# Performance work log

Measured on AMD Instinct MI355X. Metric: run time of the kernel, lower is better.

## Reference

```python
import jax, jax.numpy as jnp
import numpy as np

B, S, HID = 2, 2048, 2048
NH, NKV, HD = 32, 8, 64
N_REP = NH // NKV
SCALING = HD ** -0.5
NEG_INF = -1e9


def rotate_half(x):
    x1, x2 = x[..., : x.shape[-1] // 2], x[..., x.shape[-1] // 2 :]
    return jnp.concatenate((-x2, x1), axis=-1)


def setup_inputs() -> dict:
    key = jax.random.key(0)
    ks = jax.random.split(key, 5)
    hidden_states = jax.random.normal(ks[0], (B, S, HID), dtype=jnp.float32)
    # real RoPE tables, theta=10000
    inv_freq = 1.0 / (10000.0 ** (jnp.arange(0, HD, 2, dtype=jnp.float32) / HD))
    freqs = jnp.arange(S, dtype=jnp.float32)[:, None] * inv_freq[None, :]  # [S, HD/2]
    emb = jnp.concatenate((freqs, freqs), axis=-1)  # [S, HD]
    cos = jnp.broadcast_to(jnp.cos(emb)[None], (B, S, HD))
    sin = jnp.broadcast_to(jnp.sin(emb)[None], (B, S, HD))
    # additive causal mask [B, 1, S, S]
    causal = jnp.tril(jnp.ones((S, S), dtype=bool))
    attention_mask = jnp.where(causal, 0.0, NEG_INF).astype(jnp.float32)
    attention_mask = jnp.broadcast_to(attention_mask[None, None], (B, 1, S, S))
    std = 0.02
    Wq = jax.random.normal(ks[1], (NH * HD, HID), dtype=jnp.float32) * std
    Wk = jax.random.normal(ks[2], (NKV * HD, HID), dtype=jnp.float32) * std
    Wv = jax.random.normal(ks[3], (NKV * HD, HID), dtype=jnp.float32) * std
    Wo = jax.random.normal(ks[4], (HID, NH * HD), dtype=jnp.float32) * std
    return {"hidden_states": hidden_states, "cos": cos, "sin": sin,
            "attention_mask": attention_mask, "Wq": Wq, "Wk": Wk, "Wv": Wv, "Wo": Wo}


def reference(hidden_states, cos, sin, attention_mask, Wq, Wk, Wv, Wo):
    b, s, _ = hidden_states.shape
    # projections (nn.Linear: y = x @ W.T), split heads -> [b, h, s, d]
    q = jnp.einsum("bsh,oh->bso", hidden_states, Wq).reshape(b, s, NH, HD).transpose(0, 2, 1, 3)
    k = jnp.einsum("bsh,oh->bso", hidden_states, Wk).reshape(b, s, NKV, HD).transpose(0, 2, 1, 3)
    v = jnp.einsum("bsh,oh->bso", hidden_states, Wv).reshape(b, s, NKV, HD).transpose(0, 2, 1, 3)
    # RoPE (cos/sin unsqueezed at dim 1)
    c, sn = cos[:, None], sin[:, None]
    q = q * c + rotate_half(q) * sn
    k = k * c + rotate_half(k) * sn
    # GQA repeat_kv
    k = jnp.repeat(k, N_REP, axis=1)
    v = jnp.repeat(v, N_REP, axis=1)
    # eager attention: QK^T -> +mask -> fp32 softmax -> V
    logits = jnp.einsum("bhqd,bhkd->bhqk", q, k) * SCALING + attention_mask
    attn_weights = jax.nn.softmax(logits.astype(jnp.float32), axis=-1).astype(q.dtype)
    attn_out = jnp.einsum("bhqk,bhkd->bhqd", attn_weights, v)
    attn_out = attn_out.transpose(0, 2, 1, 3).reshape(b, s, NH * HD)
    out = jnp.einsum("bso,ho->bsh", attn_out, Wo)
    return out, attn_weights
```

## Files before the change

kernel.cpp:

```cpp
#include <hip/hip_runtime.h>
#include <hip/hip_bf16.h>


typedef __bf16 bf16;
typedef bf16 bf16x8 __attribute__((ext_vector_type(8)));
typedef bf16 bf16x4 __attribute__((ext_vector_type(4)));
typedef float f32x4 __attribute__((ext_vector_type(4)));

#define B_   2
#define S_   2048
#define HID_ 2048
#define NH_  32
#define NKV_ 8
#define HD_  64
#define TOK_ (B_*S_)
#define QKVN 3072

#define BAR_LGKM() do { asm volatile("s_waitcnt lgkmcnt(0)" ::: "memory"); \
                        __builtin_amdgcn_s_barrier(); } while (0)

__device__ __forceinline__ void gl_lds16(const bf16* g, bf16* l) {
  __builtin_amdgcn_global_load_lds(
      (const __attribute__((address_space(1))) unsigned int*)(g),
      (__attribute__((address_space(3))) unsigned int*)(l), 16, 0, 0);
}

__global__ __launch_bounds__(256) void cast_f32_bf16(const float* __restrict__ in,
                                                     bf16* __restrict__ out, int n4) {
  int i = blockIdx.x * 256 + threadIdx.x;
  if (i >= n4) return;
  f32x4 v = ((const f32x4*)in)[i];
  bf16x4 o;
  o[0] = (bf16)v[0]; o[1] = (bf16)v[1]; o[2] = (bf16)v[2]; o[3] = (bf16)v[3];
  ((bf16x4*)out)[i] = o;
}

__global__ __launch_bounds__(256) void cast_wqkv(const float* __restrict__ wq,
                                                 const float* __restrict__ wk,
                                                 const float* __restrict__ wv,
                                                 bf16* __restrict__ dst) {
  int i = blockIdx.x * 256 + threadIdx.x;
  const float* src; int off;
  if (i < 1048576)      { src = wq; off = i; }
  else if (i < 1310720) { src = wk; off = i - 1048576; }
  else                  { src = wv; off = i - 1310720; }
  f32x4 v = ((const f32x4*)src)[off];
  bf16x4 o;
  o[0] = (bf16)v[0]; o[1] = (bf16)v[1]; o[2] = (bf16)v[2]; o[3] = (bf16)v[3];
  ((bf16x4*)dst)[i] = o;
}

template<bool OUT_F32>
__global__ __launch_bounds__(256) void gemm_bt(const bf16* __restrict__ A,
                                               const bf16* __restrict__ Bm,
                                               void* __restrict__ Cout,
                                               int M, int N, int K) {
  __shared__ __align__(16) bf16 As[128 * 32];
  __shared__ __align__(16) bf16 Bs[128 * 32];
  const int tid  = threadIdx.x;
  const int wave = tid >> 6, lane = tid & 63;

  const int nwg = (int)(gridDim.x * gridDim.y);
  const int bid = (int)(blockIdx.y * gridDim.x + blockIdx.x);
  const int swz = (bid & 7) * (nwg >> 3) + (bid >> 3);
  const int bx = swz % (int)gridDim.x, by = swz / (int)gridDim.x;

  const int bm = by * 128, bn = bx * 128;
  const int wm = (wave >> 1) * 64, wn = (wave & 1) * 64;
  const int fr = lane & 15, fg = lane >> 4;

  const int r0   = wave * 32 + (lane >> 2);
  const int scol = (lane & 3) * 8;
  const bf16* ga0 = A  + (size_t)(bm + r0) * K + scol;
  const bf16* ga1 = ga0 + (size_t)16 * K;
  const bf16* gb0 = Bm + (size_t)(bn + r0) * K + scol;
  const bf16* gb1 = gb0 + (size_t)16 * K;
  bf16* lA0 = As + (wave * 32) * 32;
  bf16* lA1 = lA0 + 16 * 32;
  bf16* lB0 = Bs + (wave * 32) * 32;
  bf16* lB1 = lB0 + 16 * 32;

  f32x4 acc[4][4] = {};

  for (int k0 = 0; k0 < K; k0 += 32) {
    gl_lds16(ga0 + k0, lA0);
    gl_lds16(ga1 + k0, lA1);
    gl_lds16(gb0 + k0, lB0);
    gl_lds16(gb1 + k0, lB1);
    __syncthreads();
    bf16x8 af[4], bfv[4];
#pragma unroll
    for (int i = 0; i < 4; ++i) {
      af[i]  = *(const bf16x8*)&As[(wm + i * 16 + fr) * 32 + fg * 8];
      bfv[i] = *(const bf16x8*)&Bs[(wn + i * 16 + fr) * 32 + fg * 8];
    }
#pragma unroll
    for (int i = 0; i < 4; ++i)
#pragma unroll
      for (int j = 0; j < 4; ++j)
        acc[i][j] = __builtin_amdgcn_mfma_f32_16x16x32_bf16(af[i], bfv[j], acc[i][j], 0, 0, 0);
    __syncthreads();
  }

#pragma unroll
  for (int i = 0; i < 4; ++i)
#pragma unroll
    for (int j = 0; j < 4; ++j)
#pragma unroll
      for (int r = 0; r < 4; ++r) {
        int row = bm + wm + i * 16 + fg * 4 + r;
        int col = bn + wn + j * 16 + fr;
        float v = acc[i][j][r];
        if (OUT_F32) ((float*)Cout)[(size_t)row * N + col] = v;
        else         ((bf16*)Cout)[(size_t)row * N + col] = (bf16)v;
      }
}

__global__ __launch_bounds__(256) void rope_fused(bf16* __restrict__ qkv,
                                                  const float* __restrict__ cosp,
                                                  const float* __restrict__ sinp) {
  const int t = blockIdx.x;
  const int tid = threadIdx.x;
  const int d = tid & 31, g = tid >> 5;
  const float c = cosp[t * 64 + d];
  const float s = sinp[t * 64 + d];
  bf16* row = qkv + (size_t)t * QKVN;
#pragma unroll
  for (int i = 0; i < 4; ++i) {
    bf16* p = row + (g + i * 8) * 64 + d;
    float x1 = (float)p[0], x2 = (float)p[32];
    p[0]  = (bf16)(x1 * c - x2 * s);
    p[32] = (bf16)(x2 * c + x1 * s);
  }
  bf16* p = row + 2048 + g * 64 + d;
  float x1 = (float)p[0], x2 = (float)p[32];
  p[0]  = (bf16)(x1 * c - x2 * s);
  p[32] = (bf16)(x2 * c + x1 * s);
}

__global__ __launch_bounds__(256) void transpose_v(const bf16* __restrict__ v,
                                                   bf16* __restrict__ vT) {
  __shared__ __align__(16) bf16 t[64][72];
  const int bkv = blockIdx.y;
  const int b = bkv >> 3, kv = bkv & 7;
  const int s0 = blockIdx.x * 64;
  const int tid = threadIdx.x;
  const int r = tid >> 3, c = (tid & 7) * 8;
#pragma unroll
  for (int p = 0; p < 2; ++p) {
    int rr = r + p * 32;
    *(bf16x8*)&t[rr][c] = *(const bf16x8*)&v[(size_t)(b * S_ + s0 + rr) * QKVN + kv * 64 + c];
  }
  __syncthreads();
#pragma unroll
  for (int p = 0; p < 2; ++p) {
    int d = r + p * 32;
    bf16x8 o;
#pragma unroll
    for (int j = 0; j < 8; ++j) o[j] = t[c + j][d];
    *(bf16x8*)&vT[((size_t)bkv * 64 + d) * S_ + s0 + c] = o;
  }
}

__global__ __launch_bounds__(256, 4) void attn_kernel(const bf16* __restrict__ qkv,
                                                      const bf16* __restrict__ vT,
                                                      float* __restrict__ attnw,
                                                      bf16* __restrict__ attn_out)
{
  __shared__ __align__(16) bf16 Ks2[2][64][72];
  __shared__ __align__(16) bf16 Vs[64][72];
  __shared__ __align__(16) bf16 Ps[4][16][72];

  const int tid  = threadIdx.x;
  const int wave = tid >> 6, lane = tid & 63;
  const int qt = blockIdx.x;
  const int bh = blockIdx.y;
  const int b = bh >> 5, h = bh & 31, kv = h >> 2;
  const int qLo = qt * 64;
  const int qHi = (31 - qt) * 64;
  const int NT  = 32 - qt;
  const int fr = lane & 15, fg = lane >> 4;
  const int rw = wave * 16;
  const int rt = rw + fg * 4;
  const int thr = rw + fr;

  const int lr = tid >> 2;
  const int lc = (tid & 3) * 16;
  const bf16* kbase = qkv + (size_t)(b * S_) * QKVN + 2048 + kv * 64;
  const bf16* vbase = vT + (size_t)(b * NKV_ + kv) * 64 * S_;
  const bf16* kst = kbase + (size_t)lr * QKVN + lc;
  const bf16* vst = vbase + (size_t)lr * S_ + lc;

  bf16x8 kr0 = *(const bf16x8*)(kst);
  bf16x8 kr1 = *(const bf16x8*)(kst + 8);

  bf16x8 aqL[2], aqH[2];
  {
    const bf16* qp = qkv + (size_t)(b * S_ + qLo + rw + fr) * QKVN + h * 64 + fg * 8;
    aqL[0] = *(const bf16x8*)qp;  aqL[1] = *(const bf16x8*)(qp + 32);
    qp = qkv + (size_t)(b * S_ + qHi + rw + fr) * QKVN + h * 64 + fg * 8;
    aqH[0] = *(const bf16x8*)qp;  aqH[1] = *(const bf16x8*)(qp + 32);
  }

  {
    f32x4 z4 = {0.f, 0.f, 0.f, 0.f};
    const int zLo = (qt + 1) * 64;
    for (int rr = 0; rr < 16; ++rr) {
      size_t base = ((size_t)bh * S_ + qLo + rw + rr) * S_;
      for (int c = zLo + lane * 4; c < S_; c += 256)
        __builtin_nontemporal_store(z4, (f32x4*)&attnw[base + c]);
    }
    const int zHi = NT * 64;
    for (int rr = 0; rr < 16; ++rr) {
      size_t base = ((size_t)bh * S_ + qHi + rw + rr) * S_;
      for (int c = zHi + lane * 4; c < S_; c += 256)
        __builtin_nontemporal_store(z4, (f32x4*)&attnw[base + c]);
    }
  }

  float rsL = 0.f, rsH = 0.f;
  {
    *(bf16x8*)&Ks2[0][lr][lc]     = kr0;
    *(bf16x8*)&Ks2[0][lr][lc + 8] = kr1;
    BAR_LGKM();
    for (int jt = 0; jt < NT; ++jt) {
      const int cur = jt & 1;
      if (jt + 1 < NT) {
        const bf16* p = kst + (size_t)(jt + 1) * 64 * QKVN;
        kr0 = *(const bf16x8*)(p);
        kr1 = *(const bf16x8*)(p + 8);
      }
      {
        f32x4 acc[4] = {};
#pragma unroll
        for (int nn = 0; nn < 4; ++nn) {
          bf16x8 bk0 = *(const bf16x8*)&Ks2[cur][nn*16 + fr][fg*8];
          bf16x8 bk1 = *(const bf16x8*)&Ks2[cur][nn*16 + fr][32 + fg*8];
          acc[nn] = __builtin_amdgcn_mfma_f32_16x16x32_bf16(bk0, aqH[0], acc[nn], 0, 0, 0);
          acc[nn] = __builtin_amdgcn_mfma_f32_16x16x32_bf16(bk1, aqH[1], acc[nn], 0, 0, 0);
        }
        if (jt < NT - 1) {
#pragma unroll
          for (int nn = 0; nn < 4; ++nn)
#pragma unroll
            for (int r = 0; r < 4; ++r) rsH += __expf(acc[nn][r] * 0.125f);
        } else {
#pragma unroll
          for (int nn = 0; nn < 4; ++nn)
#pragma unroll
            for (int r = 0; r < 4; ++r)
              if (nn * 16 + fg * 4 + r <= thr) rsH += __expf(acc[nn][r] * 0.125f);
        }
      }
      if (jt <= qt) {
        f32x4 acc[4] = {};
#pragma unroll
        for (int nn = 0; nn < 4; ++nn) {
          bf16x8 bk0 = *(const bf16x8*)&Ks2[cur][nn*16 + fr][fg*8];
          bf16x8 bk1 = *(const bf16x8*)&Ks2[cur][nn*16 + fr][32 + fg*8];
          acc[nn] = __builtin_amdgcn_mfma_f32_16x16x32_bf16(bk0, aqL[0], acc[nn], 0, 0, 0);
          acc[nn] = __builtin_amdgcn_mfma_f32_16x16x32_bf16(bk1, aqL[1], acc[nn], 0, 0, 0);
        }
        if (jt < qt) {
#pragma unroll
          for (int nn = 0; nn < 4; ++nn)
#pragma unroll
            for (int r = 0; r < 4; ++r) rsL += __expf(acc[nn][r] * 0.125f);
        } else {
#pragma unroll
          for (int nn = 0; nn < 4; ++nn)
#pragma unroll
            for (int r = 0; r < 4; ++r)
              if (nn * 16 + fg * 4 + r <= thr) rsL += __expf(acc[nn][r] * 0.125f);
        }
      }
      if (jt + 1 < NT) {
        *(bf16x8*)&Ks2[cur ^ 1][lr][lc]     = kr0;
        *(bf16x8*)&Ks2[cur ^ 1][lr][lc + 8] = kr1;
        BAR_LGKM();
      }
    }
  }
  {
    float v = rsL;
    v += __shfl_xor(v, 16); v += __shfl_xor(v, 32);
    rsL = 1.0f / v;
    v = rsH;
    v += __shfl_xor(v, 16); v += __shfl_xor(v, 32);
    rsH = 1.0f / v;
  }

  f32x4 oL[4] = {}, oH[4] = {};
  {
    float* awpL = attnw + ((size_t)bh * S_ + qLo + rw + fr) * S_;
    float* awpH = attnw + ((size_t)bh * S_ + qHi + rw + fr) * S_;
    const int cb = fg * 4;
    kr0 = *(const bf16x8*)(kst);
    kr1 = *(const bf16x8*)(kst + 8);
    bf16x8 vr0 = *(const bf16x8*)(vst);
    bf16x8 vr1 = *(const bf16x8*)(vst + 8);
    for (int jt = 0; jt < NT; ++jt) {
      const int j0 = jt * 64;
      BAR_LGKM();
      *(bf16x8*)&Ks2[0][lr][lc]     = kr0;
      *(bf16x8*)&Ks2[0][lr][lc + 8] = kr1;
      *(bf16x8*)&Vs[lr][lc]     = vr0;
      *(bf16x8*)&Vs[lr][lc + 8] = vr1;
      BAR_LGKM();
      if (jt + 1 < NT) {
        const bf16* p = kst + (size_t)(jt + 1) * 64 * QKVN;
        kr0 = *(const bf16x8*)(p);
        kr1 = *(const bf16x8*)(p + 8);
        p = vst + (size_t)(jt + 1) * 64;
        vr0 = *(const bf16x8*)(p);
        vr1 = *(const bf16x8*)(p + 8);
      }
      {
        f32x4 acc[4] = {};
#pragma unroll
        for (int nn = 0; nn < 4; ++nn) {
          bf16x8 bk0 = *(const bf16x8*)&Ks2[0][nn*16 + fr][fg*8];
          bf16x8 bk1 = *(const bf16x8*)&Ks2[0][nn*16 + fr][32 + fg*8];
          acc[nn] = __builtin_amdgcn_mfma_f32_16x16x32_bf16(bk0, aqH[0], acc[nn], 0, 0, 0);
          acc[nn] = __builtin_amdgcn_mfma_f32_16x16x32_bf16(bk1, aqH[1], acc[nn], 0, 0, 0);
        }
        const bool diag = (jt == NT - 1);
#pragma unroll
        for (int nn = 0; nn < 4; ++nn) {
          f32x4 pv;
          bf16x4 pb;
#pragma unroll
          for (int r = 0; r < 4; ++r) {
            float e = __expf(acc[nn][r] * 0.125f) * rsH;
            pv[r] = (diag && (nn * 16 + cb + r > thr)) ? 0.f : e;
            pb[r] = (bf16)pv[r];
          }
          *(f32x4*)&awpH[j0 + nn * 16 + cb] = pv;
          *(bf16x4*)&Ps[wave][fr][nn * 16 + cb] = pb;
        }
        bf16x8 pa0 = *(const bf16x8*)&Ps[wave][fr][fg * 8];
        bf16x8 pa1 = *(const bf16x8*)&Ps[wave][fr][32 + fg * 8];
#pragma unroll
        for (int nn = 0; nn < 4; ++nn) {
          bf16x8 bv0 = *(const bf16x8*)&Vs[nn*16 + fr][fg*8];
          bf16x8 bv1 = *(const bf16x8*)&Vs[nn*16 + fr][32 + fg*8];
          oH[nn] = __builtin_amdgcn_mfma_f32_16x16x32_bf16(pa0, bv0, oH[nn], 0, 0, 0);
          oH[nn] = __builtin_amdgcn_mfma_f32_16x16x32_bf16(pa1, bv1, oH[nn], 0, 0, 0);
        }
      }
      if (jt <= qt) {
        f32x4 acc[4] = {};
#pragma unroll
        for (int nn = 0; nn < 4; ++nn) {
          bf16x8 bk0 = *(const bf16x8*)&Ks2[0][nn*16 + fr][fg*8];
          bf16x8 bk1 = *(const bf16x8*)&Ks2[0][nn*16 + fr][32 + fg*8];
          acc[nn] = __builtin_amdgcn_mfma_f32_16x16x32_bf16(bk0, aqL[0], acc[nn], 0, 0, 0);
          acc[nn] = __builtin_amdgcn_mfma_f32_16x16x32_bf16(bk1, aqL[1], acc[nn], 0, 0, 0);
        }
        const bool diag = (jt == qt);
#pragma unroll
        for (int nn = 0; nn < 4; ++nn) {
          f32x4 pv;
          bf16x4 pb;
#pragma unroll
          for (int r = 0; r < 4; ++r) {
            float e = __expf(acc[nn][r] * 0.125f) * rsL;
            pv[r] = (diag && (nn * 16 + cb + r > thr)) ? 0.f : e;
            pb[r] = (bf16)pv[r];
          }
          *(f32x4*)&awpL[j0 + nn * 16 + cb] = pv;
          *(bf16x4*)&Ps[wave][fr][nn * 16 + cb] = pb;
        }
        bf16x8 pa0 = *(const bf16x8*)&Ps[wave][fr][fg * 8];
        bf16x8 pa1 = *(const bf16x8*)&Ps[wave][fr][32 + fg * 8];
#pragma unroll
        for (int nn = 0; nn < 4; ++nn) {
          bf16x8 bv0 = *(const bf16x8*)&Vs[nn*16 + fr][fg*8];
          bf16x8 bv1 = *(const bf16x8*)&Vs[nn*16 + fr][32 + fg*8];
          oL[nn] = __builtin_amdgcn_mfma_f32_16x16x32_bf16(pa0, bv0, oL[nn], 0, 0, 0);
          oL[nn] = __builtin_amdgcn_mfma_f32_16x16x32_bf16(pa1, bv1, oL[nn], 0, 0, 0);
        }
      }
    }
  }

#pragma unroll
  for (int nn = 0; nn < 4; ++nn)
#pragma unroll
    for (int r = 0; r < 4; ++r) {
      int rowL = qLo + rt + r;
      int rowH = qHi + rt + r;
      attn_out[(size_t)(b * S_ + rowL) * (NH_*HD_) + h * 64 + nn * 16 + fr] = (bf16)oL[nn][r];
      attn_out[(size_t)(b * S_ + rowH) * (NH_*HD_) + h * 64 + nn * 16 + fr] = (bf16)oH[nn][r];
    }
}

extern "C" void kernel_launch(void* const* d_in, const int* in_sizes, int n_in,
                              void* d_out, int out_size, void* d_ws, size_t ws_size,
                              hipStream_t stream) {
  const float* hs   = (const float*)d_in[0];
  const float* cosp = (const float*)d_in[1];
  const float* sinp = (const float*)d_in[2];
  const float* Wq = (const float*)d_in[4];
  const float* Wk = (const float*)d_in[5];
  const float* Wv = (const float*)d_in[6];
  const float* Wo = (const float*)d_in[7];

  char* ws = (char*)d_ws;
  bf16* hs_b   = (bf16*)(ws);
  bf16* qkv_b  = (bf16*)(ws + (16u << 20));
  bf16* vT_b   = (bf16*)(ws + (40u << 20));
  bf16* ao_b   = (bf16*)(ws + (44u << 20));
  bf16* Wqkv_b = (bf16*)(ws + (60u << 20));
  bf16* Wo_b   = (bf16*)(ws + (72u << 20));

  float* outp  = (float*)d_out;
  float* attnw = outp + (size_t)TOK_ * HID_;

  cast_f32_bf16<<<(TOK_*HID_/4 + 255)/256, 256, 0, stream>>>(hs, hs_b, TOK_*HID_/4);
  cast_wqkv<<<(1572864 + 255)/256, 256, 0, stream>>>(Wq, Wk, Wv, Wqkv_b);
  cast_f32_bf16<<<(HID_*NH_*HD_/4 + 255)/256, 256, 0, stream>>>(Wo, Wo_b, HID_*NH_*HD_/4);

  gemm_bt<false><<<dim3(QKVN/128, TOK_/128), 256, 0, stream>>>(hs_b, Wqkv_b, qkv_b, TOK_, QKVN, HID_);

  rope_fused<<<TOK_, 256, 0, stream>>>(qkv_b, cosp, sinp);

  transpose_v<<<dim3(S_/64, B_*NKV_), 256, 0, stream>>>(qkv_b + 2560, vT_b);

  attn_kernel<<<dim3(S_/128, B_*NH_), 256, 0, stream>>>(qkv_b, vT_b, attnw, ao_b);

  gemm_bt<true><<<dim3(HID_/128, TOK_/128), 256, 0, stream>>>(ao_b, Wo_b, outp, TOK_, HID_, HID_);
}
```

Measured before the change: 433.3 us.

## Replace projection GEMMs with 256x256-tile triple-buffered 512-thread kernel

Both projection GEMMs move to a new kernel with 256x256 output tiles, 8 waves and 8x4 MFMA fragments per wave. It triple-buffers the K-steps in LDS with global_load_lds prefetch two steps ahead, and synchronises on partial vmcnt waits instead of full syncthreads. It also adds an XOR swizzle on the LDS layout, with matching lane remapping, and raises wave priority around the MFMA block. The aim is more reuse per loaded byte and overlap of loads with math. The larger tiles cut the grid to 192 and 128 workgroups, which may leave many CUs idle on a 256-CU part.

```diff
diff --git a/kernel.cpp b/kernel.cpp
--- a/kernel.cpp
+++ b/kernel.cpp
@@ -51,12 +51,12 @@
 }
 
 template<bool OUT_F32>
-__global__ __launch_bounds__(256) void gemm_bt(const bf16* __restrict__ A,
-                                               const bf16* __restrict__ Bm,
-                                               void* __restrict__ Cout,
-                                               int M, int N, int K) {
-  __shared__ __align__(16) bf16 As[128 * 32];
-  __shared__ __align__(16) bf16 Bs[128 * 32];
+__global__ __launch_bounds__(512, 2) void gemm256(const bf16* __restrict__ A,
+                                                  const bf16* __restrict__ Bm,
+                                                  void* __restrict__ Cout,
+                                                  int M, int N, int K) {
+  __shared__ __align__(16) bf16 sA[3][256 * 32];
+  __shared__ __align__(16) bf16 sB[3][256 * 32];
   const int tid  = threadIdx.x;
   const int wave = tid >> 6, lane = tid & 63;
 
@@ -64,53 +64,87 @@
   const int bid = (int)(blockIdx.y * gridDim.x + blockIdx.x);
   const int swz = (bid & 7) * (nwg >> 3) + (bid >> 3);
   const int bx = swz % (int)gridDim.x, by = swz / (int)gridDim.x;
-
-  const int bm = by * 128, bn = bx * 128;
-  const int wm = (wave >> 1) * 64, wn = (wave & 1) * 64;
+  const int bm = by * 256, bn = bx * 256;
+
+  const int wmi = wave >> 2, wni = wave & 3;
   const int fr = lane & 15, fg = lane >> 4;
 
-  const int r0   = wave * 32 + (lane >> 2);
-  const int scol = (lane & 3) * 8;
-  const bf16* ga0 = A  + (size_t)(bm + r0) * K + scol;
-  const bf16* ga1 = ga0 + (size_t)16 * K;
-  const bf16* gb0 = Bm + (size_t)(bn + r0) * K + scol;
-  const bf16* gb1 = gb0 + (size_t)16 * K;
-  bf16* lA0 = As + (wave * 32) * 32;
-  bf16* lA1 = lA0 + 16 * 32;
-  bf16* lB0 = Bs + (wave * 32) * 32;
-  bf16* lB1 = lB0 + 16 * 32;
-
-  f32x4 acc[4][4] = {};
-
-  for (int k0 = 0; k0 < K; k0 += 32) {
-    gl_lds16(ga0 + k0, lA0);
-    gl_lds16(ga1 + k0, lA1);
-    gl_lds16(gb0 + k0, lB0);
-    gl_lds16(gb1 + k0, lB1);
-    __syncthreads();
-    bf16x8 af[4], bfv[4];
-#pragma unroll
-    for (int i = 0; i < 4; ++i) {
-      af[i]  = *(const bf16x8*)&As[(wm + i * 16 + fr) * 32 + fg * 8];
-      bfv[i] = *(const bf16x8*)&Bs[(wn + i * 16 + fr) * 32 + fg * 8];
-    }
-#pragma unroll
-    for (int i = 0; i < 4; ++i)
-#pragma unroll
-      for (int j = 0; j < 4; ++j)
-        acc[i][j] = __builtin_amdgcn_mfma_f32_16x16x32_bf16(af[i], bfv[j], acc[i][j], 0, 0, 0);
-    __syncthreads();
-  }
-
-#pragma unroll
-  for (int i = 0; i < 4; ++i)
-#pragma unroll
-    for (int j = 0; j < 4; ++j)
+  const int lp = (lane < 32) ? lane : (lane ^ 2);
+  const int tt = (wave << 6) | lp;
+  const int srow = tt >> 2;
+  const int scol = (tt & 3) * 8;
+  const bf16* gA = A  + (size_t)(bm + srow) * K + scol;
+  const bf16* gB = Bm + (size_t)(bn + srow) * K + scol;
+  bf16* ldA = &sA[0][0] + wave * 512;
+  bf16* ldB = &sB[0][0] + wave * 512;
+
+  int aOff[8], bOff[4];
+#pragma unroll
+  for (int m = 0; m < 8; ++m) {
+    int L = (m * 16 + fr) * 64 + fg * 16;
+    L ^= ((L >> 9) & 1) << 5;
+    aOff[m] = wmi * 4096 + (L >> 1);
+  }
+#pragma unroll
+  for (int n = 0; n < 4; ++n) {
+    int rh = (wni & 1) * 64 + n * 16 + fr;
+    int L = rh * 64 + fg * 16;
+    L ^= ((L >> 9) & 1) << 5;
+    bOff[n] = (wni >> 1) * 4096 + (L >> 1);
+  }
+
+  f32x4 acc[8][4] = {};
+  const int NT = K >> 5;
+
+  auto stage = [&](int t, int buf) {
+    const bf16* ga = gA + (size_t)t * 32;
+    const bf16* gb = gB + (size_t)t * 32;
+    gl_lds16(ga,                   ldA + buf * 8192);
+    gl_lds16(ga + (size_t)128 * K, ldA + buf * 8192 + 4096);
+    gl_lds16(gb,                   ldB + buf * 8192);
+    gl_lds16(gb + (size_t)128 * K, ldB + buf * 8192 + 4096);
+  };
+
+  stage(0, 0);
+  stage(1, 1);
+  asm volatile("s_waitcnt vmcnt(4)" ::: "memory");
+  __builtin_amdgcn_s_barrier();
+
+  int ct = 0, st = 2;
+  for (int t = 0; t < NT; ++t) {
+    if (t + 2 < NT) stage(t + 2, st);
+
+    bf16x8 af[8], bfv[4];
+#pragma unroll
+    for (int m = 0; m < 8; ++m) af[m] = *(const bf16x8*)&sA[ct][aOff[m]];
+#pragma unroll
+    for (int n = 0; n < 4; ++n) bfv[n] = *(const bf16x8*)&sB[ct][bOff[n]];
+
+    __builtin_amdgcn_s_setprio(1);
+#pragma unroll
+    for (int m = 0; m < 8; ++m)
+#pragma unroll
+      for (int n = 0; n < 4; ++n)
+        acc[m][n] = __builtin_amdgcn_mfma_f32_16x16x32_bf16(af[m], bfv[n], acc[m][n], 0, 0, 0);
+    __builtin_amdgcn_s_setprio(0);
+
+    if (t + 2 < NT)      asm volatile("s_waitcnt vmcnt(4)" ::: "memory");
+    else if (t + 1 < NT) asm volatile("s_waitcnt vmcnt(0)" ::: "memory");
+    __builtin_amdgcn_s_barrier();
+
+    ct = (ct == 2) ? 0 : ct + 1;
+    st = (st == 2) ? 0 : st + 1;
+  }
+
+#pragma unroll
+  for (int m = 0; m < 8; ++m)
+#pragma unroll
+    for (int n = 0; n < 4; ++n)
 #pragma unroll
       for (int r = 0; r < 4; ++r) {
-        int row = bm + wm + i * 16 + fg * 4 + r;
-        int col = bn + wn + j * 16 + fr;
-        float v = acc[i][j][r];
+        int row = bm + wmi * 128 + m * 16 + fg * 4 + r;
+        int col = bn + wni * 64 + n * 16 + fr;
+        float v = acc[m][n][r];
         if (OUT_F32) ((float*)Cout)[(size_t)row * N + col] = v;
         else         ((bf16*)Cout)[(size_t)row * N + col] = (bf16)v;
       }
@@ -421,7 +455,7 @@
   cast_wqkv<<<(1572864 + 255)/256, 256, 0, stream>>>(Wq, Wk, Wv, Wqkv_b);
   cast_f32_bf16<<<(HID_*NH_*HD_/4 + 255)/256, 256, 0, stream>>>(Wo, Wo_b, HID_*NH_*HD_/4);
 
-  gemm_bt<false><<<dim3(QKVN/128, TOK_/128), 256, 0, stream>>>(hs_b, Wqkv_b, qkv_b, TOK_, QKVN, HID_);
+  gemm256<false><<<dim3(QKVN/256, TOK_/256), 512, 0, stream>>>(hs_b, Wqkv_b, qkv_b, TOK_, QKVN, HID_);
 
   rope_fused<<<TOK_, 256, 0, stream>>>(qkv_b, cosp, sinp);
 
@@ -429,5 +463,5 @@
 
   attn_kernel<<<dim3(S_/128, B_*NH_), 256, 0, stream>>>(qkv_b, vT_b, attnw, ao_b);
 
-  gemm_bt<true><<<dim3(HID_/128, TOK_/128), 256, 0, stream>>>(ao_b, Wo_b, outp, TOK_, HID_, HID_);
-}
+  gemm256<true><<<dim3(HID_/256, TOK_/256), 512, 0, stream>>>(ao_b, Wo_b, outp, TOK_, HID_, HID_);
+}
```

New measurement: 464.0 us. 7.1% more time.

## Fuse RoPE into QKV GEMM epilogue, merge cast kernels, nontemporal attn-weight stores

Applied to the files above, without the earlier changes.

Applies RoPE directly in the QKV projection GEMM epilogue for Q and K columns, which removes the separate rope kernel and its read-modify-write pass over qkv. The three cast kernels are merged into one launch. The attention-weight stores become nontemporal so the large fp32 probability output does not pollute the cache. The epilogue now does scalar cos/sin loads per row inside the GEMM, which could add some latency there.

```diff
diff --git a/kernel.cpp b/kernel.cpp
--- a/kernel.cpp
+++ b/kernel.cpp
@@ -25,36 +25,34 @@
       (__attribute__((address_space(3))) unsigned int*)(l), 16, 0, 0);
 }
 
-__global__ __launch_bounds__(256) void cast_f32_bf16(const float* __restrict__ in,
-                                                     bf16* __restrict__ out, int n4) {
+__global__ __launch_bounds__(256) void cast_all(const float* __restrict__ hs,
+                                                const float* __restrict__ wq,
+                                                const float* __restrict__ wk,
+                                                const float* __restrict__ wv,
+                                                const float* __restrict__ wo,
+                                                bf16* __restrict__ hs_b,
+                                                bf16* __restrict__ wqkv_b,
+                                                bf16* __restrict__ wo_b) {
   int i = blockIdx.x * 256 + threadIdx.x;
-  if (i >= n4) return;
-  f32x4 v = ((const f32x4*)in)[i];
-  bf16x4 o;
-  o[0] = (bf16)v[0]; o[1] = (bf16)v[1]; o[2] = (bf16)v[2]; o[3] = (bf16)v[3];
-  ((bf16x4*)out)[i] = o;
-}
-
-__global__ __launch_bounds__(256) void cast_wqkv(const float* __restrict__ wq,
-                                                 const float* __restrict__ wk,
-                                                 const float* __restrict__ wv,
-                                                 bf16* __restrict__ dst) {
-  int i = blockIdx.x * 256 + threadIdx.x;
-  const float* src; int off;
-  if (i < 1048576)      { src = wq; off = i; }
-  else if (i < 1310720) { src = wk; off = i - 1048576; }
-  else                  { src = wv; off = i - 1310720; }
+  const float* src; bf16* dstb; int off;
+  if (i < 2097152)      { src = hs; dstb = hs_b;                       off = i; }
+  else if (i < 3145728) { src = wq; dstb = wqkv_b;                     off = i - 2097152; }
+  else if (i < 3407872) { src = wk; dstb = wqkv_b + (size_t)4194304;   off = i - 3145728; }
+  else if (i < 3670016) { src = wv; dstb = wqkv_b + (size_t)5242880;   off = i - 3407872; }
+  else                  { src = wo; dstb = wo_b;                       off = i - 3670016; }
   f32x4 v = ((const f32x4*)src)[off];
   bf16x4 o;
   o[0] = (bf16)v[0]; o[1] = (bf16)v[1]; o[2] = (bf16)v[2]; o[3] = (bf16)v[3];
-  ((bf16x4*)dst)[i] = o;
-}
-
-template<bool OUT_F32>
+  ((bf16x4*)dstb)[off] = o;
+}
+
+template<bool OUT_F32, bool ROPE>
 __global__ __launch_bounds__(256) void gemm_bt(const bf16* __restrict__ A,
                                                const bf16* __restrict__ Bm,
                                                void* __restrict__ Cout,
-                                               int M, int N, int K) {
+                                               int M, int N, int K,
+                                               const float* __restrict__ cosp,
+                                               const float* __restrict__ sinp) {
   __shared__ __align__(16) bf16 As[128 * 32];
   __shared__ __align__(16) bf16 Bs[128 * 32];
   const int tid  = threadIdx.x;
@@ -102,40 +100,39 @@
     __syncthreads();
   }
 
-#pragma unroll
-  for (int i = 0; i < 4; ++i)
-#pragma unroll
-    for (int j = 0; j < 4; ++j)
+  if (ROPE && (bn + wn) < 2560) {
+    const int hcol = bn + wn;
+#pragma unroll
+    for (int i = 0; i < 4; ++i)
 #pragma unroll
       for (int r = 0; r < 4; ++r) {
-        int row = bm + wm + i * 16 + fg * 4 + r;
-        int col = bn + wn + j * 16 + fr;
-        float v = acc[i][j][r];
-        if (OUT_F32) ((float*)Cout)[(size_t)row * N + col] = v;
-        else         ((bf16*)Cout)[(size_t)row * N + col] = (bf16)v;
-      }
-}
-
-__global__ __launch_bounds__(256) void rope_fused(bf16* __restrict__ qkv,
-                                                  const float* __restrict__ cosp,
-                                                  const float* __restrict__ sinp) {
-  const int t = blockIdx.x;
-  const int tid = threadIdx.x;
-  const int d = tid & 31, g = tid >> 5;
-  const float c = cosp[t * 64 + d];
-  const float s = sinp[t * 64 + d];
-  bf16* row = qkv + (size_t)t * QKVN;
-#pragma unroll
-  for (int i = 0; i < 4; ++i) {
-    bf16* p = row + (g + i * 8) * 64 + d;
-    float x1 = (float)p[0], x2 = (float)p[32];
-    p[0]  = (bf16)(x1 * c - x2 * s);
-    p[32] = (bf16)(x2 * c + x1 * s);
-  }
-  bf16* p = row + 2048 + g * 64 + d;
-  float x1 = (float)p[0], x2 = (float)p[32];
-  p[0]  = (bf16)(x1 * c - x2 * s);
-  p[32] = (bf16)(x2 * c + x1 * s);
+        const int row = bm + wm + i * 16 + fg * 4 + r;
+        const float* cp = cosp + (size_t)row * 64;
+        const float* sp = sinp + (size_t)row * 64;
+        bf16* outr = (bf16*)Cout + (size_t)row * N + hcol;
+#pragma unroll
+        for (int j = 0; j < 2; ++j) {
+          const int d = j * 16 + fr;
+          const float c = cp[d], s = sp[d];
+          const float x1 = acc[i][j][r], x2 = acc[i][j + 2][r];
+          outr[d]      = (bf16)(x1 * c - x2 * s);
+          outr[d + 32] = (bf16)(x2 * c + x1 * s);
+        }
+      }
+  } else {
+#pragma unroll
+    for (int i = 0; i < 4; ++i)
+#pragma unroll
+      for (int j = 0; j < 4; ++j)
+#pragma unroll
+        for (int r = 0; r < 4; ++r) {
+          int row = bm + wm + i * 16 + fg * 4 + r;
+          int col = bn + wn + j * 16 + fr;
+          float v = acc[i][j][r];
+          if (OUT_F32) ((float*)Cout)[(size_t)row * N + col] = v;
+          else         ((bf16*)Cout)[(size_t)row * N + col] = (bf16)v;
+        }
+  }
 }
 
 __global__ __launch_bounds__(256) void transpose_v(const bf16* __restrict__ v,
@@ -335,7 +332,7 @@
             pv[r] = (diag && (nn * 16 + cb + r > thr)) ? 0.f : e;
             pb[r] = (bf16)pv[r];
           }
-          *(f32x4*)&awpH[j0 + nn * 16 + cb] = pv;
+          __builtin_nontemporal_store(pv, (f32x4*)&awpH[j0 + nn * 16 + cb]);
           *(bf16x4*)&Ps[wave][fr][nn * 16 + cb] = pb;
         }
         bf16x8 pa0 = *(const bf16x8*)&Ps[wave][fr][fg * 8];
@@ -368,7 +365,7 @@
             pv[r] = (diag && (nn * 16 + cb + r > thr)) ? 0.f : e;
             pb[r] = (bf16)pv[r];
           }
-          *(f32x4*)&awpL[j0 + nn * 16 + cb] = pv;
+          __builtin_nontemporal_store(pv, (f32x4*)&awpL[j0 + nn * 16 + cb]);
           *(bf16x4*)&Ps[wave][fr][nn * 16 + cb] = pb;
         }
         bf16x8 pa0 = *(const bf16x8*)&Ps[wave][fr][fg * 8];
@@ -417,17 +414,16 @@
   float* outp  = (float*)d_out;
   float* attnw = outp + (size_t)TOK_ * HID_;
 
-  cast_f32_bf16<<<(TOK_*HID_/4 + 255)/256, 256, 0, stream>>>(hs, hs_b, TOK_*HID_/4);
-  cast_wqkv<<<(1572864 + 255)/256, 256, 0, stream>>>(Wq, Wk, Wv, Wqkv_b);
-  cast_f32_bf16<<<(HID_*NH_*HD_/4 + 255)/256, 256, 0, stream>>>(Wo, Wo_b, HID_*NH_*HD_/4);
-
-  gemm_bt<false><<<dim3(QKVN/128, TOK_/128), 256, 0, stream>>>(hs_b, Wqkv_b, qkv_b, TOK_, QKVN, HID_);
-
-  rope_fused<<<TOK_, 256, 0, stream>>>(qkv_b, cosp, sinp);
+  cast_all<<<(4718592 + 255)/256, 256, 0, stream>>>(hs, Wq, Wk, Wv, Wo,
+                                                    hs_b, Wqkv_b, Wo_b);
+
+  gemm_bt<false, true><<<dim3(QKVN/128, TOK_/128), 256, 0, stream>>>(
+      hs_b, Wqkv_b, qkv_b, TOK_, QKVN, HID_, cosp, sinp);
 
   transpose_v<<<dim3(S_/64, B_*NKV_), 256, 0, stream>>>(qkv_b + 2560, vT_b);
 
   attn_kernel<<<dim3(S_/128, B_*NH_), 256, 0, stream>>>(qkv_b, vT_b, attnw, ao_b);
 
-  gemm_bt<true><<<dim3(HID_/128, TOK_/128), 256, 0, stream>>>(ao_b, Wo_b, outp, TOK_, HID_, HID_);
-}
+  gemm_bt<true, false><<<dim3(HID_/128, TOK_/128), 256, 0, stream>>>(
+      ao_b, Wo_b, outp, TOK_, HID_, HID_, nullptr, nullptr);
+}
```

Measured after the change: 499.2 us. 15.2% more time.
